# Optimization experiments

Hardware: AMD Instinct MI355X
Metric: run time of the kernel (lower is better)

The kernel has to match this reference:

```python
import jax, jax.numpy as jnp
import numpy as np

M = 64      # memory_size
DV = 64     # memory_value_state_dim
DK = 64     # memory_key_state_dim
DQA = 128   # qa_embed_dim
B = 16384


def setup_inputs() -> dict:
    key = jax.random.key(0)
    ks = jax.random.split(key, 16)
    s = 0.05
    return {
        'control_key': jax.random.normal(ks[0], (B, DK), jnp.float32),
        'control_qa': jax.random.normal(ks[1], (B, DQA), jnp.float32),
        'memory_key': jax.random.normal(ks[2], (M, DK), jnp.float32),
        'memory_value': jax.random.normal(ks[3], (B, M, DV), jnp.float32),
        'We': jax.random.normal(ks[4], (DQA, DV), jnp.float32) * s,
        'be': jnp.zeros((DV,), jnp.float32),
        'Wemv': jax.random.normal(ks[5], (M * DV, DV), jnp.float32) * s,
        'bemv': jnp.zeros((DV,), jnp.float32),
        'Wza': jax.random.normal(ks[6], (DV, DV), jnp.float32) * s,
        'bza': jnp.zeros((DV,), jnp.float32),
        'Wamv': jax.random.normal(ks[7], (M * DV, DV), jnp.float32) * s,
        'bamv': jnp.zeros((DV,), jnp.float32),
        'Wc0': jax.random.normal(ks[8], (M * DV, DQA), jnp.float32) * s,
        'bc0': jnp.zeros((DQA,), jnp.float32),
        'Wm1': jax.random.normal(ks[9], (DQA, M * DV), jnp.float32) * s,
        'bm1': jnp.zeros((M * DV,), jnp.float32),
        'Wz': jax.random.normal(ks[10], (DQA, DV), jnp.float32) * s,
        'bz': jnp.zeros((DV,), jnp.float32),
        'Wzmv': jax.random.normal(ks[11], (M * DV, DV), jnp.float32) * s,
        'bzmv': jnp.zeros((DV,), jnp.float32),
    }


def reference(control_key, control_qa, memory_key, memory_value,
              We, be, Wemv, bemv, Wza, bza, Wamv, bamv,
              Wc0, bc0, Wm1, bm1, Wz, bz, Wzmv, bzmv):
    # attention: log_softmax(control_key @ memory_key^T).exp() == softmax
    write_weight = jax.nn.softmax(control_key @ memory_key.T, axis=1)  # [B, M]

    # ---- hyper_write ----
    mem_flat0 = memory_value.reshape(-1, M * DV)                       # [B, M*DV]
    # content_m_round0: Flatten -> Linear -> Sigmoid, gated by control_qa
    content0 = control_qa * jax.nn.sigmoid(mem_flat0 @ Wc0 + bc0)      # [B, DQA]
    # memory_m_round1 gating of memory
    gate1 = jax.nn.sigmoid(content0 @ Wm1 + bm1).reshape(-1, M, DV)
    memory_pre = memory_value * gate1                                  # [B, M, DV]
    mem_flat = memory_pre.reshape(-1, M * DV)

    # erase: sigmoid(erase_net(content0) + erase_mv_net(flat(memory_pre)))
    erase_signal = jax.nn.sigmoid(
        jax.nn.sigmoid(content0 @ We + be)
        + jax.nn.sigmoid(mem_flat @ Wemv + bemv))                      # [B, DV]

    # zt: sigmoid(zt_signal(content0) + zt_signal_Mv(flat(memory_pre)))
    zt = jax.nn.sigmoid((content0 @ Wz + bz) + (mem_flat @ Wzmv + bzmv))

    # add: tanh(zt_add_net(zt) + add_mv_net(flat(memory_pre)))
    add_signal = jnp.tanh(
        jnp.tanh(zt @ Wza + bza) + jnp.tanh(mem_flat @ Wamv + bamv))   # [B, DV]

    # outer-product erase/add update
    w = write_weight[:, :, None]                                       # [B, M, 1]
    erase_mult = 1.0 - w * erase_signal[:, None, :]                     # [B, M, DV]
    aggre_add = w * add_signal[:, None, :]
    new_memory = memory_pre * erase_mult + aggre_add                    # [B, M, DV]
    return new_memory


if __name__ == '__main__':
    out = reference(**setup_inputs())
    print(out.shape)
```

## Files before the change

kernel.cpp:

```cpp
#include <hip/hip_runtime.h>

#define NB  16384
#define MM  64
#define DV  64
#define DK  64
#define DQA 128
#define MD  4096
#define LDW 4224

typedef float  floatx4 __attribute__((ext_vector_type(4)));
typedef short  shortx8 __attribute__((ext_vector_type(8)));
typedef unsigned short ushortx4 __attribute__((ext_vector_type(4)));

static __device__ __forceinline__ unsigned short f2bf(float f) {
  union { float f; unsigned int u; } v; v.f = f;
  unsigned int r = v.u + 0x7FFFu + ((v.u >> 16) & 1u);
  return (unsigned short)(r >> 16);
}
static __device__ __forceinline__ float bf2f(unsigned short u) {
  union { unsigned int u; float f; } v; v.u = (unsigned int)u << 16; return v.f;
}
static __device__ __forceinline__ float sigm(float x) { return 1.0f / (1.0f + __expf(-x)); }

static __device__ __forceinline__ shortx8 load8bf(const float* p) {
  const float4* p4 = (const float4*)p;
  float4 a = p4[0];
  float4 b = p4[1];
  shortx8 r;
  r[0] = (short)f2bf(a.x); r[1] = (short)f2bf(a.y);
  r[2] = (short)f2bf(a.z); r[3] = (short)f2bf(a.w);
  r[4] = (short)f2bf(b.x); r[5] = (short)f2bf(b.y);
  r[6] = (short)f2bf(b.z); r[7] = (short)f2bf(b.w);
  return r;
}

__global__ __launch_bounds__(256) void k_tr(const float* __restrict__ src,
                                            unsigned short* __restrict__ dst,
                                            int N, int dstld) {
  __shared__ unsigned short T[64 * 72];
  const int k0 = blockIdx.x * 64, n0 = blockIdx.y * 64;
  const int t = threadIdx.x;
#pragma unroll
  for (int i = 0; i < 16; ++i) {
    int idx = t + i * 256, kl = idx >> 6, nl = idx & 63;
    T[kl * 72 + nl] = f2bf(src[(size_t)(k0 + kl) * N + n0 + nl]);
  }
  __syncthreads();
#pragma unroll
  for (int i = 0; i < 16; ++i) {
    int idx = t + i * 256, nl = idx >> 6, kl = idx & 63;
    dst[(size_t)(n0 + nl) * dstld + k0 + kl] = T[kl * 72 + nl];
  }
}

__global__ __launch_bounds__(256) void k_ww(const float* __restrict__ ck,
                                            const float* __restrict__ mk,
                                            float* __restrict__ ww) {
  const int t = threadIdx.x;
  const int lane = t & 63;
  const int wv = t >> 6;
  const int b = blockIdx.x * 4 + wv;
  const float4* ck4 = (const float4*)(ck + (size_t)b * DK);
  const float4* mk4 = (const float4*)(mk + (size_t)lane * DK);
  float s = 0.f;
#pragma unroll
  for (int i = 0; i < DK / 4; ++i) {
    float4 a = ck4[i], m = mk4[i];
    s += a.x * m.x + a.y * m.y + a.z * m.z + a.w * m.w;
  }
  float mx = s;
#pragma unroll
  for (int off = 32; off; off >>= 1) mx = fmaxf(mx, __shfl_xor(mx, off, 64));
  float e = __expf(s - mx);
  float sum = e;
#pragma unroll
  for (int off = 32; off; off >>= 1) sum += __shfl_xor(sum, off, 64);
  ww[(size_t)b * MM + lane] = e / sum;
}

__global__ __launch_bounds__(256) void k_c0(const float* __restrict__ mv,
                                            const unsigned short* __restrict__ WcT,
                                            float* __restrict__ P) {
  __shared__ __align__(16) unsigned short WB[DQA * 136];
  const int t = threadIdx.x, lane = t & 63, wv = t >> 6;
  const int quad = lane >> 4, l16 = lane & 15;
  const int mh = wv & 1, nq2 = wv >> 1;
  const int rowbase = blockIdx.x * 32;
  const int split = blockIdx.y;
  const int arow = rowbase + mh * 16 + l16;

  floatx4 acc[4];
#pragma unroll
  for (int nt = 0; nt < 4; ++nt) acc[nt] = (floatx4){0.f, 0.f, 0.f, 0.f};

  for (int c = 0; c < 16; ++c) {
    const int kc = split * 16 + ((c + blockIdx.x) & 15);
    const int kb = kc * 128;
    shortx8 afr[4];
#pragma unroll
    for (int ks = 0; ks < 4; ++ks)
      afr[ks] = load8bf(mv + (size_t)arow * MD + kb + ks * 32 + quad * 8);
#pragma unroll
    for (int i = 0; i < 8; ++i) {
      int idx = t + i * 256;
      int n = idx >> 4, kbk = idx & 15;
      *(shortx8*)&WB[n * 136 + kbk * 8] =
          *(const shortx8*)(WcT + (size_t)n * LDW + kb + kbk * 8);
    }
    __syncthreads();
#pragma unroll
    for (int nt = 0; nt < 4; ++nt)
#pragma unroll
      for (int ks = 0; ks < 4; ++ks) {
        shortx8 bfr = *(const shortx8*)&WB[(nq2 * 64 + nt * 16 + l16) * 136 + ks * 32 + quad * 8];
        acc[nt] = __builtin_amdgcn_mfma_f32_16x16x32_bf16(afr[ks], bfr, acc[nt], 0, 0, 0);
      }
    __syncthreads();
  }
  float* Pp = P + (size_t)split * NB * DQA;
#pragma unroll
  for (int nt = 0; nt < 4; ++nt) {
    int col = nq2 * 64 + nt * 16 + l16;
#pragma unroll
    for (int r = 0; r < 4; ++r) {
      int row = rowbase + mh * 16 + quad * 4 + r;
      Pp[(size_t)row * DQA + col] = acc[nt][r];
    }
  }
}

__global__ __launch_bounds__(256) void k_c0fin(const float* __restrict__ P,
                                               const float* __restrict__ bc0,
                                               const float* __restrict__ qa,
                                               unsigned short* __restrict__ c0p) {
  const size_t i4 = ((size_t)blockIdx.x * 256 + threadIdx.x) * 4;
  const int col = (int)(i4 & (DQA - 1));
  float4 p0 = *(const float4*)(P + i4);
  float4 p1 = *(const float4*)(P + (size_t)NB * DQA + i4);
  float4 b  = *(const float4*)(bc0 + col);
  float4 q  = *(const float4*)(qa + i4);
  ushortx4 o;
  o[0] = f2bf(q.x * sigm(p0.x + p1.x + b.x));
  o[1] = f2bf(q.y * sigm(p0.y + p1.y + b.y));
  o[2] = f2bf(q.z * sigm(p0.z + p1.z + b.z));
  o[3] = f2bf(q.w * sigm(p0.w + p1.w + b.w));
  *(ushortx4*)(c0p + i4) = o;
}

__global__ __launch_bounds__(256) void k_g1mp(const float* __restrict__ mv,
                                              const unsigned short* __restrict__ c0p,
                                              const unsigned short* __restrict__ Wm1T,
                                              const float* __restrict__ bm1,
                                              float* __restrict__ mp) {
  __shared__ __align__(16) unsigned short WB[128 * 136];
  const int t = threadIdx.x, lane = t & 63, wv = t >> 6;
  const int quad = lane >> 4, l16 = lane & 15;
  const int rowbase = blockIdx.x * 64;
  const int colbase = blockIdx.y * 128;

  shortx8 c0fr[4];
#pragma unroll
  for (int ks = 0; ks < 4; ++ks)
    c0fr[ks] = *(const shortx8*)(c0p + (size_t)(rowbase + wv * 16 + l16) * DQA + ks * 32 + quad * 8);

#pragma unroll
  for (int i = 0; i < 8; ++i) {
    int idx = t + i * 256;
    int n = idx >> 4, kbk = idx & 15;
    *(shortx8*)&WB[n * 136 + kbk * 8] =
        *(const shortx8*)(Wm1T + (size_t)(colbase + n) * DQA + kbk * 8);
  }
  __syncthreads();

  floatx4 acc[8];
#pragma unroll
  for (int nt = 0; nt < 8; ++nt) acc[nt] = (floatx4){0.f, 0.f, 0.f, 0.f};
#pragma unroll
  for (int nt = 0; nt < 8; ++nt)
#pragma unroll
    for (int ks = 0; ks < 4; ++ks) {
      shortx8 bfr = *(const shortx8*)&WB[(nt * 16 + l16) * 136 + ks * 32 + quad * 8];
      acc[nt] = __builtin_amdgcn_mfma_f32_16x16x32_bf16(c0fr[ks], bfr, acc[nt], 0, 0, 0);
    }

#pragma unroll
  for (int nt = 0; nt < 8; ++nt) {
    int colg = colbase + nt * 16 + l16;
    float b = bm1[colg];
#pragma unroll
    for (int r = 0; r < 4; ++r) {
      int row = rowbase + wv * 16 + quad * 4 + r;
      float g = sigm(acc[nt][r] + b);
      mp[(size_t)row * MD + colg] = mv[(size_t)row * MD + colg] * g;
    }
  }
}

__global__ __launch_bounds__(256) void k_S(const float* __restrict__ mp,
                                           const unsigned short* __restrict__ W3T,
                                           float* __restrict__ Sg) {
  __shared__ __align__(16) unsigned short WB[192 * 136];
  const int t = threadIdx.x, lane = t & 63, wv = t >> 6;
  const int quad = lane >> 4, l16 = lane & 15;
  const int mh = wv & 1, nh2 = wv >> 1;
  const int rowbase = blockIdx.x * 32;
  const int split = blockIdx.y;
  const int arow = rowbase + mh * 16 + l16;

  floatx4 acc[6];
#pragma unroll
  for (int nt = 0; nt < 6; ++nt) acc[nt] = (floatx4){0.f, 0.f, 0.f, 0.f};

  for (int c = 0; c < 16; ++c) {
    const int kc = split * 16 + ((c + blockIdx.x) & 15);
    const int kb = kc * 128;
    shortx8 afr[4];
#pragma unroll
    for (int ks = 0; ks < 4; ++ks)
      afr[ks] = load8bf(mp + (size_t)arow * MD + kb + ks * 32 + quad * 8);
#pragma unroll
    for (int i = 0; i < 12; ++i) {
      int idx = t + i * 256;
      int n = idx >> 4, kbk = idx & 15;
      *(shortx8*)&WB[n * 136 + kbk * 8] =
          *(const shortx8*)(W3T + (size_t)n * LDW + kb + kbk * 8);
    }
    __syncthreads();
#pragma unroll
    for (int nt = 0; nt < 6; ++nt)
#pragma unroll
      for (int ks = 0; ks < 4; ++ks) {
        shortx8 bfr = *(const shortx8*)&WB[(nh2 * 96 + nt * 16 + l16) * 136 + ks * 32 + quad * 8];
        acc[nt] = __builtin_amdgcn_mfma_f32_16x16x32_bf16(afr[ks], bfr, acc[nt], 0, 0, 0);
      }
    __syncthreads();
  }
  float* Sp = Sg + (size_t)split * NB * 192;
#pragma unroll
  for (int nt = 0; nt < 6; ++nt) {
    int col = nh2 * 96 + nt * 16 + l16;
#pragma unroll
    for (int r = 0; r < 4; ++r) {
      int row = rowbase + mh * 16 + quad * 4 + r;
      Sp[(size_t)row * 192 + col] = acc[nt][r];
    }
  }
}

__global__ __launch_bounds__(256) void k_eza(const unsigned short* __restrict__ c0p,
                                             const float* __restrict__ Sg,
                                             const float* __restrict__ We,
                                             const float* __restrict__ be,
                                             const float* __restrict__ Wz,
                                             const float* __restrict__ bz,
                                             const float* __restrict__ Wza,
                                             const float* __restrict__ bza,
                                             const float* __restrict__ bemv,
                                             const float* __restrict__ bzmv,
                                             const float* __restrict__ bamv,
                                             float* __restrict__ eg,
                                             float* __restrict__ ag) {
  __shared__ float ztl[4][64];
  const int t = threadIdx.x;
  const int j = t & 63;
  const int r = t >> 6;
  const int b = blockIdx.x * 4 + r;
  const unsigned short* c0r = c0p + (size_t)b * DQA;
  float ae = 0.f, az = 0.f;
#pragma unroll 8
  for (int k = 0; k < DQA; ++k) {
    float cv = bf2f(c0r[k]);
    ae += cv * We[k * DV + j];
    az += cv * Wz[k * DV + j];
  }
  const float* Sr0 = Sg + (size_t)b * 192;
  const float* Sr1 = Sg + (size_t)NB * 192 + (size_t)b * 192;
  float zt = sigm(az + bz[j] + Sr0[64 + j] + Sr1[64 + j] + bzmv[j]);
  ztl[r][j] = zt;
  __syncthreads();
  float aa = 0.f;
#pragma unroll 8
  for (int k = 0; k < DV; ++k) aa += ztl[r][k] * Wza[k * DV + j];
  float aval = tanhf(tanhf(aa + bza[j]) + tanhf(Sr0[128 + j] + Sr1[128 + j] + bamv[j]));
  float eval = sigm(sigm(ae + be[j]) + sigm(Sr0[j] + Sr1[j] + bemv[j]));
  eg[(size_t)b * DV + j] = eval;
  ag[(size_t)b * DV + j] = aval;
}

__global__ __launch_bounds__(256) void k_final(float* __restrict__ mp,
                                               const float* __restrict__ ww,
                                               const float* __restrict__ eg,
                                               const float* __restrict__ ag) {
  const size_t idx8 = ((size_t)blockIdx.x * 256 + threadIdx.x) * 8;
  const int row = (int)(idx8 >> 12);
  const int colg = (int)(idx8 & 4095);
  const int mi = colg >> 6, j = colg & 63;
  const float w = ww[(size_t)row * MM + mi];
  const float4 e0 = *(const float4*)(eg + (size_t)row * DV + j);
  const float4 e1 = *(const float4*)(eg + (size_t)row * DV + j + 4);
  const float4 a0 = *(const float4*)(ag + (size_t)row * DV + j);
  const float4 a1 = *(const float4*)(ag + (size_t)row * DV + j + 4);
  float4 m0 = *(const float4*)(mp + idx8);
  float4 m1 = *(const float4*)(mp + idx8 + 4);
  m0.x = m0.x * (1.f - w * e0.x) + w * a0.x;
  m0.y = m0.y * (1.f - w * e0.y) + w * a0.y;
  m0.z = m0.z * (1.f - w * e0.z) + w * a0.z;
  m0.w = m0.w * (1.f - w * e0.w) + w * a0.w;
  m1.x = m1.x * (1.f - w * e1.x) + w * a1.x;
  m1.y = m1.y * (1.f - w * e1.y) + w * a1.y;
  m1.z = m1.z * (1.f - w * e1.z) + w * a1.z;
  m1.w = m1.w * (1.f - w * e1.w) + w * a1.w;
  *(float4*)(mp + idx8) = m0;
  *(float4*)(mp + idx8 + 4) = m1;
}

extern "C" void kernel_launch(void* const* d_in, const int* in_sizes, int n_in,
                              void* d_out, int out_size, void* d_ws, size_t ws_size,
                              hipStream_t stream) {
  const float* ck   = (const float*)d_in[0];
  const float* qa   = (const float*)d_in[1];
  const float* mk   = (const float*)d_in[2];
  const float* mv   = (const float*)d_in[3];
  const float* We   = (const float*)d_in[4];
  const float* be   = (const float*)d_in[5];
  const float* Wemv = (const float*)d_in[6];
  const float* bemv = (const float*)d_in[7];
  const float* Wza  = (const float*)d_in[8];
  const float* bza  = (const float*)d_in[9];
  const float* Wamv = (const float*)d_in[10];
  const float* bamv = (const float*)d_in[11];
  const float* Wc0  = (const float*)d_in[12];
  const float* bc0  = (const float*)d_in[13];
  const float* Wm1  = (const float*)d_in[14];
  const float* bm1  = (const float*)d_in[15];
  const float* Wz   = (const float*)d_in[16];
  const float* bz   = (const float*)d_in[17];
  const float* Wzmv = (const float*)d_in[18];
  const float* bzmv = (const float*)d_in[19];
  float* outp = (float*)d_out;

  char* base = (char*)d_ws;
  float* wwp = (float*)base;                      base += (size_t)NB * MM * 4;
  unsigned short* c0p = (unsigned short*)base;    base += (size_t)NB * DQA * 2;
  float* Sp = (float*)base;                       base += (size_t)2 * NB * 192 * 4;
  float* ep = (float*)base;                       base += (size_t)NB * DV * 4;
  float* ap = (float*)base;                       base += (size_t)NB * DV * 4;
  unsigned short* WcT  = (unsigned short*)base;   base += (size_t)DQA * LDW * 2;
  unsigned short* Wm1T = (unsigned short*)base;   base += (size_t)MD * DQA * 2;
  unsigned short* W3T  = (unsigned short*)base;   base += (size_t)192 * LDW * 2;

  float* Pp = outp;

  k_tr<<<dim3(MD / 64, DQA / 64), 256, 0, stream>>>(Wc0, WcT, DQA, LDW);
  k_tr<<<dim3(DQA / 64, MD / 64), 256, 0, stream>>>(Wm1, Wm1T, MD, DQA);
  k_tr<<<dim3(MD / 64, 1), 256, 0, stream>>>(Wemv, W3T, DV, LDW);
  k_tr<<<dim3(MD / 64, 1), 256, 0, stream>>>(Wzmv, W3T + (size_t)64 * LDW, DV, LDW);
  k_tr<<<dim3(MD / 64, 1), 256, 0, stream>>>(Wamv, W3T + (size_t)128 * LDW, DV, LDW);

  k_ww<<<NB / 4, 256, 0, stream>>>(ck, mk, wwp);
  k_c0<<<dim3(NB / 32, 2), 256, 0, stream>>>(mv, WcT, Pp);
  k_c0fin<<<(NB * DQA / 4) / 256, 256, 0, stream>>>(Pp, bc0, qa, c0p);
  k_g1mp<<<dim3(NB / 64, MD / 128), 256, 0, stream>>>(mv, c0p, Wm1T, bm1, outp);
  k_S<<<dim3(NB / 32, 2), 256, 0, stream>>>(outp, W3T, Sp);
  k_eza<<<NB / 4, 256, 0, stream>>>(c0p, Sp, We, be, Wz, bz, Wza, bza, bemv, bzmv, bamv, ep, ap);
  k_final<<<(NB * MD / 8) / 256, 256, 0, stream>>>(outp, wwp, ep, ap);
}
```

Before: 1.047 ms.

## Stage A tiles in LDS, coalesce gated-memory stores, emit bf16 copy for S GEMM

k_c0 and k_S now use 512-thread blocks covering 64 rows, with the A operand loaded cooperatively as coalesced float4 rows, converted to bf16 and staged in LDS. Previously each lane made strided per-row loads. k_g1mp transposes its accumulators through LDS so the sigmoid-gated memory is written with coalesced float4 stores. When the workspace is large enough it also writes a bf16 copy of the gated memory, which k_S reads instead of the fp32 version, halving the A-side traffic there. The cost is the extra bf16 write and more LDS per block, which may reduce occupancy.

```diff
diff --git a/kernel.cpp b/kernel.cpp
--- a/kernel.cpp
+++ b/kernel.cpp
@@ -21,18 +21,6 @@
   union { unsigned int u; float f; } v; v.u = (unsigned int)u << 16; return v.f;
 }
 static __device__ __forceinline__ float sigm(float x) { return 1.0f / (1.0f + __expf(-x)); }
-
-static __device__ __forceinline__ shortx8 load8bf(const float* p) {
-  const float4* p4 = (const float4*)p;
-  float4 a = p4[0];
-  float4 b = p4[1];
-  shortx8 r;
-  r[0] = (short)f2bf(a.x); r[1] = (short)f2bf(a.y);
-  r[2] = (short)f2bf(a.z); r[3] = (short)f2bf(a.w);
-  r[4] = (short)f2bf(b.x); r[5] = (short)f2bf(b.y);
-  r[6] = (short)f2bf(b.z); r[7] = (short)f2bf(b.w);
-  return r;
-}
 
 __global__ __launch_bounds__(256) void k_tr(const float* __restrict__ src,
                                             unsigned short* __restrict__ dst,
@@ -78,16 +66,16 @@
   ww[(size_t)b * MM + lane] = e / sum;
 }
 
-__global__ __launch_bounds__(256) void k_c0(const float* __restrict__ mv,
-                                            const unsigned short* __restrict__ WcT,
-                                            float* __restrict__ P) {
+__global__ __launch_bounds__(512, 4) void k_c0(const float* __restrict__ mv,
+                                               const unsigned short* __restrict__ WcT,
+                                               float* __restrict__ P) {
   __shared__ __align__(16) unsigned short WB[DQA * 136];
+  __shared__ __align__(16) unsigned short AB[64 * 136];
   const int t = threadIdx.x, lane = t & 63, wv = t >> 6;
   const int quad = lane >> 4, l16 = lane & 15;
-  const int mh = wv & 1, nq2 = wv >> 1;
-  const int rowbase = blockIdx.x * 32;
+  const int mh = wv & 3, nq = wv >> 2;
+  const int rowbase = blockIdx.x * 64;
   const int split = blockIdx.y;
-  const int arow = rowbase + mh * 16 + l16;
 
   floatx4 acc[4];
 #pragma unroll
@@ -96,23 +84,32 @@
   for (int c = 0; c < 16; ++c) {
     const int kc = split * 16 + ((c + blockIdx.x) & 15);
     const int kb = kc * 128;
-    shortx8 afr[4];
-#pragma unroll
-    for (int ks = 0; ks < 4; ++ks)
-      afr[ks] = load8bf(mv + (size_t)arow * MD + kb + ks * 32 + quad * 8);
-#pragma unroll
-    for (int i = 0; i < 8; ++i) {
-      int idx = t + i * 256;
+#pragma unroll
+    for (int p = 0; p < 4; ++p) {
+      int row = p * 16 + (t >> 5);
+      int col4 = (t & 31) * 4;
+      float4 v = *(const float4*)(mv + (size_t)(rowbase + row) * MD + kb + col4);
+      ushortx4 o;
+      o[0] = f2bf(v.x); o[1] = f2bf(v.y); o[2] = f2bf(v.z); o[3] = f2bf(v.w);
+      *(ushortx4*)&AB[row * 136 + col4] = o;
+    }
+#pragma unroll
+    for (int p = 0; p < 4; ++p) {
+      int idx = t + p * 512;
       int n = idx >> 4, kbk = idx & 15;
       *(shortx8*)&WB[n * 136 + kbk * 8] =
           *(const shortx8*)(WcT + (size_t)n * LDW + kb + kbk * 8);
     }
     __syncthreads();
+    shortx8 afr[4];
+#pragma unroll
+    for (int ks = 0; ks < 4; ++ks)
+      afr[ks] = *(const shortx8*)&AB[(mh * 16 + l16) * 136 + ks * 32 + quad * 8];
 #pragma unroll
     for (int nt = 0; nt < 4; ++nt)
 #pragma unroll
       for (int ks = 0; ks < 4; ++ks) {
-        shortx8 bfr = *(const shortx8*)&WB[(nq2 * 64 + nt * 16 + l16) * 136 + ks * 32 + quad * 8];
+        shortx8 bfr = *(const shortx8*)&WB[(nq * 64 + nt * 16 + l16) * 136 + ks * 32 + quad * 8];
         acc[nt] = __builtin_amdgcn_mfma_f32_16x16x32_bf16(afr[ks], bfr, acc[nt], 0, 0, 0);
       }
     __syncthreads();
@@ -120,7 +117,7 @@
   float* Pp = P + (size_t)split * NB * DQA;
 #pragma unroll
   for (int nt = 0; nt < 4; ++nt) {
-    int col = nq2 * 64 + nt * 16 + l16;
+    int col = nq * 64 + nt * 16 + l16;
 #pragma unroll
     for (int r = 0; r < 4; ++r) {
       int row = rowbase + mh * 16 + quad * 4 + r;
@@ -151,8 +148,12 @@
                                               const unsigned short* __restrict__ c0p,
                                               const unsigned short* __restrict__ Wm1T,
                                               const float* __restrict__ bm1,
-                                              float* __restrict__ mp) {
-  __shared__ __align__(16) unsigned short WB[128 * 136];
+                                              float* __restrict__ mp,
+                                              unsigned short* __restrict__ mpb,
+                                              int usebf) {
+  __shared__ __align__(16) unsigned char SM[128 * 136 * 2];
+  unsigned short* WB = (unsigned short*)SM;
+  float* Tf = (float*)SM;
   const int t = threadIdx.x, lane = t & 63, wv = t >> 6;
   const int quad = lane >> 4, l16 = lane & 15;
   const int rowbase = blockIdx.x * 64;
@@ -183,29 +184,54 @@
       acc[nt] = __builtin_amdgcn_mfma_f32_16x16x32_bf16(c0fr[ks], bfr, acc[nt], 0, 0, 0);
     }
 
-#pragma unroll
-  for (int nt = 0; nt < 8; ++nt) {
-    int colg = colbase + nt * 16 + l16;
-    float b = bm1[colg];
-#pragma unroll
-    for (int r = 0; r < 4; ++r) {
-      int row = rowbase + wv * 16 + quad * 4 + r;
-      float g = sigm(acc[nt][r] + b);
-      mp[(size_t)row * MD + colg] = mv[(size_t)row * MD + colg] * g;
-    }
-  }
-}
-
-__global__ __launch_bounds__(256) void k_S(const float* __restrict__ mp,
-                                           const unsigned short* __restrict__ W3T,
-                                           float* __restrict__ Sg) {
+  __syncthreads();
+#pragma unroll
+  for (int nt = 0; nt < 8; ++nt)
+#pragma unroll
+    for (int r = 0; r < 4; ++r)
+      Tf[(wv * 16 + quad * 4 + r) * 132 + nt * 16 + l16] = acc[nt][r];
+  __syncthreads();
+
+  const int row = t >> 2;
+  const int colq = (t & 3) * 32;
+  const float* mvp = mv + (size_t)(rowbase + row) * MD + colbase + colq;
+  float* mpp = mp + (size_t)(rowbase + row) * MD + colbase + colq;
+  const float* bmp = bm1 + colbase + colq;
+  unsigned short tb[32];
+#pragma unroll
+  for (int i = 0; i < 8; ++i) {
+    float4 g4 = *(const float4*)&Tf[row * 132 + colq + i * 4];
+    float4 b4 = *(const float4*)(bmp + i * 4);
+    float4 m4 = *(const float4*)(mvp + i * 4);
+    float4 o;
+    o.x = m4.x * sigm(g4.x + b4.x);
+    o.y = m4.y * sigm(g4.y + b4.y);
+    o.z = m4.z * sigm(g4.z + b4.z);
+    o.w = m4.w * sigm(g4.w + b4.w);
+    *(float4*)(mpp + i * 4) = o;
+    tb[i * 4 + 0] = f2bf(o.x); tb[i * 4 + 1] = f2bf(o.y);
+    tb[i * 4 + 2] = f2bf(o.z); tb[i * 4 + 3] = f2bf(o.w);
+  }
+  if (usebf) {
+    unsigned short* mbp = mpb + (size_t)(rowbase + row) * LDW + colbase + colq;
+#pragma unroll
+    for (int j = 0; j < 4; ++j)
+      *(shortx8*)(mbp + j * 8) = *(const shortx8*)&tb[j * 8];
+  }
+}
+
+__global__ __launch_bounds__(512, 4) void k_S(const float* __restrict__ mp32,
+                                              const unsigned short* __restrict__ mpb,
+                                              const unsigned short* __restrict__ W3T,
+                                              float* __restrict__ Sg,
+                                              int usebf) {
   __shared__ __align__(16) unsigned short WB[192 * 136];
+  __shared__ __align__(16) unsigned short AB[64 * 136];
   const int t = threadIdx.x, lane = t & 63, wv = t >> 6;
   const int quad = lane >> 4, l16 = lane & 15;
-  const int mh = wv & 1, nh2 = wv >> 1;
-  const int rowbase = blockIdx.x * 32;
+  const int mh = wv & 3, nh = wv >> 2;
+  const int rowbase = blockIdx.x * 64;
   const int split = blockIdx.y;
-  const int arow = rowbase + mh * 16 + l16;
 
   floatx4 acc[6];
 #pragma unroll
@@ -214,23 +240,42 @@
   for (int c = 0; c < 16; ++c) {
     const int kc = split * 16 + ((c + blockIdx.x) & 15);
     const int kb = kc * 128;
-    shortx8 afr[4];
-#pragma unroll
-    for (int ks = 0; ks < 4; ++ks)
-      afr[ks] = load8bf(mp + (size_t)arow * MD + kb + ks * 32 + quad * 8);
-#pragma unroll
-    for (int i = 0; i < 12; ++i) {
-      int idx = t + i * 256;
+    if (usebf) {
+#pragma unroll
+      for (int p = 0; p < 2; ++p) {
+        int row = p * 32 + (t >> 4);
+        int col8 = (t & 15) * 8;
+        *(shortx8*)&AB[row * 136 + col8] =
+            *(const shortx8*)(mpb + (size_t)(rowbase + row) * LDW + kb + col8);
+      }
+    } else {
+#pragma unroll
+      for (int p = 0; p < 4; ++p) {
+        int row = p * 16 + (t >> 5);
+        int col4 = (t & 31) * 4;
+        float4 v = *(const float4*)(mp32 + (size_t)(rowbase + row) * MD + kb + col4);
+        ushortx4 o;
+        o[0] = f2bf(v.x); o[1] = f2bf(v.y); o[2] = f2bf(v.z); o[3] = f2bf(v.w);
+        *(ushortx4*)&AB[row * 136 + col4] = o;
+      }
+    }
+#pragma unroll
+    for (int p = 0; p < 6; ++p) {
+      int idx = t + p * 512;
       int n = idx >> 4, kbk = idx & 15;
       *(shortx8*)&WB[n * 136 + kbk * 8] =
           *(const shortx8*)(W3T + (size_t)n * LDW + kb + kbk * 8);
     }
     __syncthreads();
+    shortx8 afr[4];
+#pragma unroll
+    for (int ks = 0; ks < 4; ++ks)
+      afr[ks] = *(const shortx8*)&AB[(mh * 16 + l16) * 136 + ks * 32 + quad * 8];
 #pragma unroll
     for (int nt = 0; nt < 6; ++nt)
 #pragma unroll
       for (int ks = 0; ks < 4; ++ks) {
-        shortx8 bfr = *(const shortx8*)&WB[(nh2 * 96 + nt * 16 + l16) * 136 + ks * 32 + quad * 8];
+        shortx8 bfr = *(const shortx8*)&WB[(nh * 96 + nt * 16 + l16) * 136 + ks * 32 + quad * 8];
         acc[nt] = __builtin_amdgcn_mfma_f32_16x16x32_bf16(afr[ks], bfr, acc[nt], 0, 0, 0);
       }
     __syncthreads();
@@ -238,7 +283,7 @@
   float* Sp = Sg + (size_t)split * NB * 192;
 #pragma unroll
   for (int nt = 0; nt < 6; ++nt) {
-    int col = nh2 * 96 + nt * 16 + l16;
+    int col = nh * 96 + nt * 16 + l16;
 #pragma unroll
     for (int r = 0; r < 4; ++r) {
       int row = rowbase + mh * 16 + quad * 4 + r;
@@ -348,6 +393,9 @@
   unsigned short* WcT  = (unsigned short*)base;   base += (size_t)DQA * LDW * 2;
   unsigned short* Wm1T = (unsigned short*)base;   base += (size_t)MD * DQA * 2;
   unsigned short* W3T  = (unsigned short*)base;   base += (size_t)192 * LDW * 2;
+  unsigned short* mpb  = (unsigned short*)base;
+  size_t needed = (size_t)(base - (char*)d_ws) + (size_t)NB * LDW * 2;
+  const int usebf = (ws_size >= needed) ? 1 : 0;
 
   float* Pp = outp;
 
@@ -358,10 +406,10 @@
   k_tr<<<dim3(MD / 64, 1), 256, 0, stream>>>(Wamv, W3T + (size_t)128 * LDW, DV, LDW);
 
   k_ww<<<NB / 4, 256, 0, stream>>>(ck, mk, wwp);
-  k_c0<<<dim3(NB / 32, 2), 256, 0, stream>>>(mv, WcT, Pp);
+  k_c0<<<dim3(NB / 64, 2), 512, 0, stream>>>(mv, WcT, Pp);
   k_c0fin<<<(NB * DQA / 4) / 256, 256, 0, stream>>>(Pp, bc0, qa, c0p);
-  k_g1mp<<<dim3(NB / 64, MD / 128), 256, 0, stream>>>(mv, c0p, Wm1T, bm1, outp);
-  k_S<<<dim3(NB / 32, 2), 256, 0, stream>>>(outp, W3T, Sp);
+  k_g1mp<<<dim3(NB / 64, MD / 128), 256, 0, stream>>>(mv, c0p, Wm1T, bm1, outp, mpb, usebf);
+  k_S<<<dim3(NB / 64, 2), 512, 0, stream>>>(outp, mpb, W3T, Sp, usebf);
   k_eza<<<NB / 4, 256, 0, stream>>>(c0p, Sp, We, be, Wz, bz, Wza, bza, bemv, bzmv, bamv, ep, ap);
   k_final<<<(NB * MD / 8) / 256, 256, 0, stream>>>(outp, wwp, ep, ap);
 }
```

Measured after the change: 1.012 ms. -3.4%, faster.
